# Optimization experiments

Hardware: AMD Instinct MI355X
Metric: run time of the kernel (lower is better)

The kernel has to match this reference:

```python
import jax, jax.numpy as jnp
import numpy as np

FS = 50000000.0
PI = jnp.pi


def _scale_matrix(alpha, kW, n_pad):
    """kW x kW matrix equal to torch linear-interp (align_corners=False)
    kW -> N -> kW with N = round(kW / clamp(alpha, 0.001)), N bounded by n_pad."""
    a = jnp.maximum(alpha, 0.001)
    N = jnp.clip(jnp.round(kW / a), 1, n_pad).astype(jnp.int32)
    Nf = N.astype(jnp.float32)
    eye_k = jnp.eye(kW, dtype=jnp.float32)
    eye_n = jnp.eye(n_pad, dtype=jnp.float32)
    # down-sample matrix D: length kW -> N (rows j >= N masked to 0)
    j = jnp.arange(n_pad, dtype=jnp.float32)
    c = jnp.maximum((j + 0.5) * (kW / Nf) - 0.5, 0.0)
    i0f = jnp.floor(c)
    w1 = c - i0f
    i0 = jnp.clip(i0f.astype(jnp.int32), 0, kW - 1)
    i1 = jnp.minimum(i0 + 1, kW - 1)
    D = (1.0 - w1)[:, None] * eye_k[i0] + w1[:, None] * eye_k[i1]
    D = D * (jnp.arange(n_pad) < N)[:, None]
    # up-sample matrix U: length N -> kW (reads only cols < N)
    i = jnp.arange(kW, dtype=jnp.float32)
    c2 = jnp.maximum((i + 0.5) * (Nf / kW) - 0.5, 0.0)
    j0 = jnp.floor(c2).astype(jnp.int32)
    j1 = jnp.minimum(j0 + 1, N - 1)
    w2 = c2 - j0.astype(jnp.float32)
    U = (1.0 - w2)[:, None] * eye_n[j0] + w2[:, None] * eye_n[j1]
    return U @ D  # [kW, kW]


def _mix_phase(w, phi):
    # w: [B,OC,2,1,kW], phi: [B,kW]; complex rotation of (I,Q) channel pair
    I, Q = w[:, :, 0, 0, :], w[:, :, 1, 0, :]
    c, sn = jnp.cos(phi)[:, None, :], jnp.sin(phi)[:, None, :]
    return jnp.stack([I * c - Q * sn, I * sn + Q * c], axis=2)[:, :, :, None, :]


def _steered_kernels(z, s, base_w, B):
    OC, IC, _, kW = base_w.shape
    n_pad = 2 * kW
    sf = jnp.nan_to_num(s)
    act = z > 0
    pick = lambda idx, neutral: jnp.where(act[:, idx], sf[:, idx], neutral)
    wB = jnp.broadcast_to(base_w[None], (B, OC, IC, 1, kW))
    # SCALE (PERTURB_ORDER idx 1)
    alpha = pick(1, 1.0)
    M = jax.vmap(lambda a: _scale_matrix(a, kW, n_pad))(alpha)  # [B,kW,kW]
    wB = jnp.einsum('bij,bocuj->bocui', M, wB)
    # CFO (idx 0) then CHIRP (idx 4): sequential phase rotations = summed phase
    n = jnp.arange(kW, dtype=jnp.float32)
    phi = 2.0 * PI * pick(0, 0.0)[:, None] * n[None, :] / FS
    t = n / FS
    phi = phi + PI * pick(4, 0.0)[:, None] * (t ** 2)[None, :]
    wB = _mix_phase(wB, phi)
    # GAIN (idx 2)
    wB = pick(2, 1.0)[:, None, None, None, None] * wB
    # SHIFT (idx 3): per-sample circular roll, out[i] = in[(i - s) mod kW]
    sh = jnp.round(pick(3, 0.0)).astype(jnp.int32)
    idx = (jnp.arange(kW)[None, :] - sh[:, None]) % kW  # [B,kW]
    idx = jnp.broadcast_to(idx[:, None, None, None, :], wB.shape)
    wB = jnp.take_along_axis(wB, idx, axis=-1)
    return wB  # [B,OC,2,1,kW]


def reference(x, z, s, base_w):
    B, IC, _, L = x.shape
    OC, _, _, kW = base_w.shape
    wB = _steered_kernels(z, s, base_w, B)
    xG = x.reshape(1, B * IC, 1, L)
    wG = wB.reshape(B * OC, IC, 1, kW)
    y = jax.lax.conv_general_dilated(
        xG, wG, window_strides=(1, 1), padding=[(0, 0), (kW // 2, kW // 2)],
        dimension_numbers=('NCHW', 'OIHW', 'NCHW'), feature_group_count=B)
    return y.reshape(B, OC, 1, L)


def setup_inputs() -> dict:
    key = jax.random.key(0)
    ks = jax.random.split(key, 4)
    B, OC, IC, kW, L = 32, 64, 2, 65, 65536
    x = jax.random.normal(ks[0], (B, IC, 1, L), dtype=jnp.float32)
    base_w = jax.random.normal(ks[1], (OC, IC, 1, kW), dtype=jnp.float32) * 0.1
    z = jax.random.randint(ks[2], (B, 5), 0, 2).astype(jnp.int32)
    u = jax.random.uniform(ks[3], (B, 5), dtype=jnp.float32)
    f0 = (u[:, 0] * 2.0 - 1.0) * 1.0e5         # CFO in +/-100 kHz
    alpha = 0.75 + u[:, 1] * 0.65               # SCALE in [0.75, 1.4]
    gain = 0.5 + u[:, 2]                        # GAIN in [0.5, 1.5]
    shift = jnp.round((u[:, 3] * 2.0 - 1.0) * 3.0)  # SHIFT integer in [-3, 3]
    chirp = (u[:, 4] * 2.0 - 1.0) * 1.0e12      # CHIRP rate
    s = jnp.stack([f0, alpha, gain, shift, chirp], axis=1)
    return {"x": x, "z": z, "s": s, "base_w": base_w}
```

## Files before the change

kernel.cpp:

```cpp
#include <hip/hip_runtime.h>
#include <math.h>

#define KW 65
#define L_LEN 65536
#define B_N 32
#define OC_N 64
#define KPAD 160
#define SEC 80
#define LT 256
#define NT 4
#define LGRP (LT*NT)
#define XBASE 344

typedef __attribute__((ext_vector_type(8))) short short8;
typedef __attribute__((ext_vector_type(4))) float f32x4;

__device__ __forceinline__ unsigned short f2bf(float f) {
    unsigned u = __builtin_bit_cast(unsigned, f);
    unsigned r = u + 0x7FFFu + ((u >> 16) & 1u);
    return (unsigned short)(r >> 16);
}

__device__ __forceinline__ float nan0(float v) {
    if (isnan(v)) return 0.0f;
    if (isinf(v)) return v > 0.0f ? 3.4028234663852886e38f : -3.4028234663852886e38f;
    return v;
}

__global__ __launch_bounds__(256) void steer_weights(
        const int* __restrict__ z, const float* __restrict__ s,
        const float* __restrict__ bw, unsigned short* __restrict__ wpk) {
    const float PI = 3.14159265358979323846f;
    const float FS = 50000000.0f;
    int b = blockIdx.x;
    int t = threadIdx.x;

    const int*   zb = z + b * 5;
    const float* sb = s + b * 5;
    float f0    = (zb[0] > 0) ? nan0(sb[0]) : 0.0f;
    float alpha = (zb[1] > 0) ? nan0(sb[1]) : 1.0f;
    float gain  = (zb[2] > 0) ? nan0(sb[2]) : 1.0f;
    float shf   = (zb[3] > 0) ? nan0(sb[3]) : 0.0f;
    float chirp = (zb[4] > 0) ? nan0(sb[4]) : 0.0f;

    float a = fmaxf(alpha, 0.001f);
    float Nf_raw = rintf(65.0f / a);
    int   N  = (int)fminf(fmaxf(Nf_raw, 1.0f), 130.0f);
    float Nf = (float)N;
    int   sh = (int)rintf(shf);

    __shared__ float rw[OC_N][2][KW];
    __shared__ float cph[KW], sph[KW];
    __shared__ int   j0t[KW], j1t[KW];
    __shared__ float w2t[KW];
    __shared__ int   i0t[130], i1t[130];
    __shared__ float w1t[130];

    if (t < KW) {
        float n  = (float)t;
        float tt = n / FS;
        float phi = 2.0f * PI * f0 * n / FS + PI * chirp * tt * tt;
        cph[t] = cosf(phi);
        sph[t] = sinf(phi);
        float c2  = fmaxf(((float)t + 0.5f) * (Nf / 65.0f) - 0.5f, 0.0f);
        float j0f = floorf(c2);
        j0t[t] = (int)j0f;
        j1t[t] = min((int)j0f + 1, N - 1);
        w2t[t] = c2 - j0f;
    } else if (t < KW + 130) {
        int j = t - KW;
        float c   = fmaxf(((float)j + 0.5f) * (65.0f / Nf) - 0.5f, 0.0f);
        float i0f = floorf(c);
        int   i0  = min((int)i0f, KW - 1);
        i0t[j] = i0;
        i1t[j] = min(i0 + 1, KW - 1);
        w1t[j] = c - i0f;
    }
    __syncthreads();

    for (int item = t; item < 128 * KW; item += 256) {
        int row = item / KW, i = item % KW;
        const float* w = bw + row * KW;
        int j0 = j0t[i], j1 = j1t[i];
        float v0 = (1.0f - w1t[j0]) * w[i0t[j0]] + w1t[j0] * w[i1t[j0]];
        float v1 = (1.0f - w1t[j1]) * w[i0t[j1]] + w1t[j1] * w[i1t[j1]];
        rw[row >> 1][row & 1][i] = (1.0f - w2t[i]) * v0 + w2t[i] * v1;
    }
    __syncthreads();

    {
        int oc = t >> 2, q = t & 3;
        unsigned short* ob = wpk + ((size_t)b * OC_N + oc) * KPAD;
        int sh0 = ((sh % KW) + KW) % KW;
        int k0 = 17 * q, k1 = min(KW, k0 + 17);
        for (int k = k0; k < k1; ++k) {
            float I = rw[oc][0][k], Q = rw[oc][1][k];
            float cp = cph[k], sp = sph[k];
            float Ip = (I * cp - Q * sp) * gain;
            float Qp = (I * sp + Q * cp) * gain;
            int kk = k + sh0; if (kk >= KW) kk -= KW;
            ob[kk]       = f2bf(Ip);
            ob[SEC + kk] = f2bf(Qp);
        }
        if (q == 3) {
            for (int kk = KW; kk < SEC; ++kk) { ob[kk] = 0; ob[SEC + kk] = 0; }
        }
    }
}

__global__ __launch_bounds__(256, 3) void steer_conv_mfma(
        const float* __restrict__ x, const unsigned short* __restrict__ wpk,
        float* __restrict__ y) {
    int b   = blockIdx.y;
    int L0  = blockIdx.x * LGRP;
    int tid = threadIdx.x;
    int wv = tid >> 6, lane = tid & 63;
    int c = lane & 15, g = lane >> 4;
    int a = wv & 1, lsub = wv >> 1;

    __shared__ __align__(16) unsigned short xt[2][8][2][XBASE];

    short8 afr[2][5];
    #pragma unroll
    for (int ot = 0; ot < 2; ++ot) {
        const unsigned short* wb = wpk + ((size_t)b * OC_N + 32 * a + 16 * ot + c) * KPAD;
        #pragma unroll
        for (int s = 0; s < 5; ++s)
            afr[ot][s] = *(const short8*)(wb + 32 * s + 8 * g);
    }

    const float* xb = x + (size_t)b * 2 * L_LEN;

    bool isLoader = (tid >= 84);
    int lidx = tid - 84;
    int lch = lidx / 86, li4 = lidx % 86;

    int boff[5];
    #pragma unroll
    for (int s = 0; s < 5; ++s) {
        int k0 = 32 * s + 8 * g;
        int ch = (k0 >= SEC) ? 1 : 0;
        int t0 = k0 - SEC * ch;
        boff[s] = ch * XBASE + 128 * lsub + 8 * c + t0;
    }

    float4 v;
    if (isLoader) {
        int gi = L0 - 32 + 4 * li4;
        if (gi >= 0 && gi + 3 < L_LEN) {
            v = *(const float4*)(xb + (size_t)lch * L_LEN + gi);
        } else {
            float tmp[4];
            #pragma unroll
            for (int u = 0; u < 4; ++u) {
                int q = gi + u;
                tmp[u] = (q >= 0 && q < L_LEN) ? xb[(size_t)lch * L_LEN + q] : 0.0f;
            }
            v = make_float4(tmp[0], tmp[1], tmp[2], tmp[3]);
        }
    }

    int cur = 0;
    for (int t = 0; t < NT; ++t) {
        int l0 = L0 + t * LT;
        if (isLoader) {
            unsigned r0 = (unsigned)f2bf(v.x) | ((unsigned)f2bf(v.y) << 16);
            unsigned r1 = (unsigned)f2bf(v.z) | ((unsigned)f2bf(v.w) << 16);
            *(uint2*)&xt[cur][0][lch][4 * li4] = make_uint2(r0, r1);
        }
        __syncthreads();
        if (tid < 84) {
            int ch = tid / 42, j = tid % 42;
            const unsigned* src = (const unsigned*)&xt[cur][0][ch][8 * j];
            unsigned d[8];
            #pragma unroll
            for (int i = 0; i < 8; ++i) d[i] = src[i];
            #pragma unroll
            for (int p = 1; p < 8; ++p) {
                int q = p >> 1;
                unsigned o[4];
                #pragma unroll
                for (int i = 0; i < 4; ++i)
                    o[i] = (p & 1) ? ((d[i + q] >> 16) | (d[i + q + 1] << 16)) : d[i + q];
                *(uint4*)&xt[cur][p][ch][8 * j] = make_uint4(o[0], o[1], o[2], o[3]);
            }
        } else if (t + 1 < NT) {
            int gi = L0 + (t + 1) * LT - 32 + 4 * li4;
            if (gi >= 0 && gi + 3 < L_LEN) {
                v = *(const float4*)(xb + (size_t)lch * L_LEN + gi);
            } else {
                float tmp[4];
                #pragma unroll
                for (int u = 0; u < 4; ++u) {
                    int q = gi + u;
                    tmp[u] = (q >= 0 && q < L_LEN) ? xb[(size_t)lch * L_LEN + q] : 0.0f;
                }
                v = make_float4(tmp[0], tmp[1], tmp[2], tmp[3]);
            }
        }
        __syncthreads();

        f32x4 acc[2][8];
        #pragma unroll
        for (int ot = 0; ot < 2; ++ot)
            #pragma unroll
            for (int p = 0; p < 8; ++p) acc[ot][p] = (f32x4){0.f, 0.f, 0.f, 0.f};

        #pragma unroll
        for (int p = 0; p < 8; ++p) {
            const unsigned short* xp = &xt[cur][p][0][0];
            #pragma unroll
            for (int s = 0; s < 5; ++s) {
                short8 bfr = *(const short8*)(xp + boff[s]);
                acc[0][p] = __builtin_amdgcn_mfma_f32_16x16x32_bf16(afr[0][s], bfr, acc[0][p], 0, 0, 0);
                acc[1][p] = __builtin_amdgcn_mfma_f32_16x16x32_bf16(afr[1][s], bfr, acc[1][p], 0, 0, 0);
            }
        }

        #pragma unroll
        for (int ot = 0; ot < 2; ++ot) {
            #pragma unroll
            for (int r = 0; r < 4; ++r) {
                int oc = 32 * a + 16 * ot + 4 * g + r;
                float* yr = y + ((size_t)b * OC_N + oc) * L_LEN + l0 + 128 * lsub + 8 * c;
                f32x4 lo = { acc[ot][0][r], acc[ot][1][r], acc[ot][2][r], acc[ot][3][r] };
                f32x4 hi = { acc[ot][4][r], acc[ot][5][r], acc[ot][6][r], acc[ot][7][r] };
                *(f32x4*)yr       = lo;
                *((f32x4*)yr + 1) = hi;
            }
        }
        cur ^= 1;
    }
}

extern "C" void kernel_launch(void* const* d_in, const int* in_sizes, int n_in,
                              void* d_out, int out_size, void* d_ws, size_t ws_size,
                              hipStream_t stream) {
    const float* x  = (const float*)d_in[0];
    const int*   z  = (const int*)d_in[1];
    const float* s  = (const float*)d_in[2];
    const float* bw = (const float*)d_in[3];
    float* y = (float*)d_out;
    unsigned short* wpk = (unsigned short*)d_ws;

    steer_weights<<<dim3(B_N), dim3(256), 0, stream>>>(z, s, bw, wpk);
    steer_conv_mfma<<<dim3(L_LEN / LGRP, B_N), dim3(256), 0, stream>>>(x, wpk, y);
}
```

Before: 142.2 us.

## Build shifted bf16 conv windows in registers instead of eight LDS copies

The conv kernel no longer stages eight pre-shifted copies of the input tile in shared memory. Each lane now loads two 16-byte chunks per K-slice and builds all eight shifted B fragments in registers with shifts and ORs. This drops the second barrier and the specialised shifter threads, and cuts LDS use enough to possibly raise occupancy. NT also doubles to 8, so each block handles twice the L range and there are half as many blocks. The cost is more VALU work and register pressure per MFMA, and fewer blocks to fill the GPU.

```diff
diff --git a/kernel.cpp b/kernel.cpp
--- a/kernel.cpp
+++ b/kernel.cpp
@@ -8,12 +8,13 @@
 #define KPAD 160
 #define SEC 80
 #define LT 256
-#define NT 4
+#define NT 8
 #define LGRP (LT*NT)
 #define XBASE 344
 
 typedef __attribute__((ext_vector_type(8))) short short8;
 typedef __attribute__((ext_vector_type(4))) float f32x4;
+typedef __attribute__((ext_vector_type(4))) unsigned u32x4;
 
 __device__ __forceinline__ unsigned short f2bf(float f) {
     unsigned u = __builtin_bit_cast(unsigned, f);
@@ -118,7 +119,7 @@
     int c = lane & 15, g = lane >> 4;
     int a = wv & 1, lsub = wv >> 1;
 
-    __shared__ __align__(16) unsigned short xt[2][8][2][XBASE];
+    __shared__ __align__(16) unsigned short xt[2][2][XBASE];
 
     short8 afr[2][5];
     #pragma unroll
@@ -131,9 +132,8 @@
 
     const float* xb = x + (size_t)b * 2 * L_LEN;
 
-    bool isLoader = (tid >= 84);
-    int lidx = tid - 84;
-    int lch = lidx / 86, li4 = lidx % 86;
+    bool isLdr = (tid < 172);
+    int lch = tid / 86, li4 = tid % 86;
 
     int boff[5];
     #pragma unroll
@@ -144,9 +144,9 @@
         boff[s] = ch * XBASE + 128 * lsub + 8 * c + t0;
     }
 
-    float4 v;
-    if (isLoader) {
-        int gi = L0 - 32 + 4 * li4;
+    auto loadwin = [&](int l0) -> float4 {
+        int gi = l0 - 32 + 4 * li4;
+        float4 v;
         if (gi >= 0 && gi + 3 < L_LEN) {
             v = *(const float4*)(xb + (size_t)lch * L_LEN + gi);
         } else {
@@ -158,60 +158,51 @@
             }
             v = make_float4(tmp[0], tmp[1], tmp[2], tmp[3]);
         }
-    }
+        return v;
+    };
+
+    float4 v = make_float4(0.f, 0.f, 0.f, 0.f);
+    if (isLdr) v = loadwin(L0);
 
     int cur = 0;
     for (int t = 0; t < NT; ++t) {
         int l0 = L0 + t * LT;
-        if (isLoader) {
+        if (isLdr) {
             unsigned r0 = (unsigned)f2bf(v.x) | ((unsigned)f2bf(v.y) << 16);
             unsigned r1 = (unsigned)f2bf(v.z) | ((unsigned)f2bf(v.w) << 16);
-            *(uint2*)&xt[cur][0][lch][4 * li4] = make_uint2(r0, r1);
+            *(uint2*)&xt[cur][lch][4 * li4] = make_uint2(r0, r1);
         }
         __syncthreads();
-        if (tid < 84) {
-            int ch = tid / 42, j = tid % 42;
-            const unsigned* src = (const unsigned*)&xt[cur][0][ch][8 * j];
-            unsigned d[8];
-            #pragma unroll
-            for (int i = 0; i < 8; ++i) d[i] = src[i];
-            #pragma unroll
-            for (int p = 1; p < 8; ++p) {
-                int q = p >> 1;
-                unsigned o[4];
-                #pragma unroll
-                for (int i = 0; i < 4; ++i)
-                    o[i] = (p & 1) ? ((d[i + q] >> 16) | (d[i + q + 1] << 16)) : d[i + q];
-                *(uint4*)&xt[cur][p][ch][8 * j] = make_uint4(o[0], o[1], o[2], o[3]);
-            }
-        } else if (t + 1 < NT) {
-            int gi = L0 + (t + 1) * LT - 32 + 4 * li4;
-            if (gi >= 0 && gi + 3 < L_LEN) {
-                v = *(const float4*)(xb + (size_t)lch * L_LEN + gi);
-            } else {
-                float tmp[4];
-                #pragma unroll
-                for (int u = 0; u < 4; ++u) {
-                    int q = gi + u;
-                    tmp[u] = (q >= 0 && q < L_LEN) ? xb[(size_t)lch * L_LEN + q] : 0.0f;
+
+        float4 vN = v;
+        if (isLdr && t + 1 < NT) vN = loadwin(l0 + LT);
+
+        f32x4 acc[2][8];
+        #pragma unroll
+        for (int ot = 0; ot < 2; ++ot)
+            #pragma unroll
+            for (int p = 0; p < 8; ++p) acc[ot][p] = (f32x4){0.f, 0.f, 0.f, 0.f};
+
+        const unsigned short* xs = &xt[cur][0][0];
+        #pragma unroll
+        for (int s = 0; s < 5; ++s) {
+            const uint4* w16 = (const uint4*)(xs + boff[s]);
+            uint4 q0 = w16[0], q1 = w16[1];
+            unsigned d[8] = { q0.x, q0.y, q0.z, q0.w, q1.x, q1.y, q1.z, q1.w };
+            #pragma unroll
+            for (int p = 0; p < 8; ++p) {
+                u32x4 ov;
+                if (p & 1) {
+                    int q = p >> 1;
+                    ov = (u32x4){ (d[q]     >> 16) | (d[q + 1] << 16),
+                                  (d[q + 1] >> 16) | (d[q + 2] << 16),
+                                  (d[q + 2] >> 16) | (d[q + 3] << 16),
+                                  (d[q + 3] >> 16) | (d[q + 4] << 16) };
+                } else {
+                    int q = p >> 1;
+                    ov = (u32x4){ d[q], d[q + 1], d[q + 2], d[q + 3] };
                 }
-                v = make_float4(tmp[0], tmp[1], tmp[2], tmp[3]);
-            }
-        }
-        __syncthreads();
-
-        f32x4 acc[2][8];
-        #pragma unroll
-        for (int ot = 0; ot < 2; ++ot)
-            #pragma unroll
-            for (int p = 0; p < 8; ++p) acc[ot][p] = (f32x4){0.f, 0.f, 0.f, 0.f};
-
-        #pragma unroll
-        for (int p = 0; p < 8; ++p) {
-            const unsigned short* xp = &xt[cur][p][0][0];
-            #pragma unroll
-            for (int s = 0; s < 5; ++s) {
-                short8 bfr = *(const short8*)(xp + boff[s]);
+                short8 bfr = __builtin_bit_cast(short8, ov);
                 acc[0][p] = __builtin_amdgcn_mfma_f32_16x16x32_bf16(afr[0][s], bfr, acc[0][p], 0, 0, 0);
                 acc[1][p] = __builtin_amdgcn_mfma_f32_16x16x32_bf16(afr[1][s], bfr, acc[1][p], 0, 0, 0);
             }
@@ -229,6 +220,7 @@
                 *((f32x4*)yr + 1) = hi;
             }
         }
+        v = vN;
         cur ^= 1;
     }
 }
```

Result: slower. 201.7 us (+41.9%).

## Parallelize weight steering over OC groups and streamline conv tile pipeline

Applied to the files above, without the earlier changes.

The weight-steering kernel is split across 8 output-channel groups per batch, so it runs on 256 blocks instead of 32. In the conv kernel each loader thread now builds all eight shifted bf16 copies directly from registers. This removes the separate shift pass and one __syncthreads per tile, and the next tile's global load is issued before the MFMA work. Output stores are split into two halves, issued mid-compute, and each block covers twice as many tiles. The cost is fewer conv blocks, which may hurt load balance, plus more register pressure in the loader threads.

```diff
diff --git a/kernel.cpp b/kernel.cpp
--- a/kernel.cpp
+++ b/kernel.cpp
@@ -8,7 +8,7 @@
 #define KPAD 160
 #define SEC 80
 #define LT 256
-#define NT 4
+#define NT 8
 #define LGRP (LT*NT)
 #define XBASE 344
 
@@ -19,6 +19,10 @@
     unsigned u = __builtin_bit_cast(unsigned, f);
     unsigned r = u + 0x7FFFu + ((u >> 16) & 1u);
     return (unsigned short)(r >> 16);
+}
+
+__device__ __forceinline__ unsigned pk2(float a, float b) {
+    return (unsigned)f2bf(a) | ((unsigned)f2bf(b) << 16);
 }
 
 __device__ __forceinline__ float nan0(float v) {
@@ -32,8 +36,9 @@
         const float* __restrict__ bw, unsigned short* __restrict__ wpk) {
     const float PI = 3.14159265358979323846f;
     const float FS = 50000000.0f;
-    int b = blockIdx.x;
-    int t = threadIdx.x;
+    int ocg = blockIdx.x;
+    int b   = blockIdx.y;
+    int t   = threadIdx.x;
 
     const int*   zb = z + b * 5;
     const float* sb = s + b * 5;
@@ -49,7 +54,7 @@
     float Nf = (float)N;
     int   sh = (int)rintf(shf);
 
-    __shared__ float rw[OC_N][2][KW];
+    __shared__ float rw[8][2][KW];
     __shared__ float cph[KW], sph[KW];
     __shared__ int   j0t[KW], j1t[KW];
     __shared__ float w2t[KW];
@@ -78,9 +83,9 @@
     }
     __syncthreads();
 
-    for (int item = t; item < 128 * KW; item += 256) {
+    for (int item = t; item < 16 * KW; item += 256) {
         int row = item / KW, i = item % KW;
-        const float* w = bw + row * KW;
+        const float* w = bw + (((ocg * 8 + (row >> 1)) * 2) + (row & 1)) * KW;
         int j0 = j0t[i], j1 = j1t[i];
         float v0 = (1.0f - w1t[j0]) * w[i0t[j0]] + w1t[j0] * w[i1t[j0]];
         float v1 = (1.0f - w1t[j1]) * w[i0t[j1]] + w1t[j1] * w[i1t[j1]];
@@ -88,23 +93,23 @@
     }
     __syncthreads();
 
-    {
-        int oc = t >> 2, q = t & 3;
-        unsigned short* ob = wpk + ((size_t)b * OC_N + oc) * KPAD;
-        int sh0 = ((sh % KW) + KW) % KW;
-        int k0 = 17 * q, k1 = min(KW, k0 + 17);
-        for (int k = k0; k < k1; ++k) {
-            float I = rw[oc][0][k], Q = rw[oc][1][k];
-            float cp = cph[k], sp = sph[k];
-            float Ip = (I * cp - Q * sp) * gain;
-            float Qp = (I * sp + Q * cp) * gain;
-            int kk = k + sh0; if (kk >= KW) kk -= KW;
-            ob[kk]       = f2bf(Ip);
-            ob[SEC + kk] = f2bf(Qp);
-        }
-        if (q == 3) {
-            for (int kk = KW; kk < SEC; ++kk) { ob[kk] = 0; ob[SEC + kk] = 0; }
-        }
+    int sh0 = ((sh % KW) + KW) % KW;
+    for (int item = t; item < 8 * KW; item += 256) {
+        int ocl = item / KW, k = item % KW;
+        unsigned short* ob = wpk + ((size_t)b * OC_N + ocg * 8 + ocl) * KPAD;
+        float I = rw[ocl][0][k], Q = rw[ocl][1][k];
+        float cp = cph[k], sp = sph[k];
+        float Ip = (I * cp - Q * sp) * gain;
+        float Qp = (I * sp + Q * cp) * gain;
+        int kk = k + sh0; if (kk >= KW) kk -= KW;
+        ob[kk]       = f2bf(Ip);
+        ob[SEC + kk] = f2bf(Qp);
+    }
+    for (int item = t; item < 8 * 30; item += 256) {
+        int ocl = item / 30, rem = item % 30;
+        int sec = rem / 15, kk = KW + rem % 15;
+        unsigned short* ob = wpk + ((size_t)b * OC_N + ocg * 8 + ocl) * KPAD;
+        ob[sec * SEC + kk] = 0;
     }
 }
 
@@ -131,9 +136,8 @@
 
     const float* xb = x + (size_t)b * 2 * L_LEN;
 
-    bool isLoader = (tid >= 84);
-    int lidx = tid - 84;
-    int lch = lidx / 86, li4 = lidx % 86;
+    bool isLdr = (tid < 86);
+    int lch = tid / 43, lj = tid % 43;
 
     int boff[5];
     #pragma unroll
@@ -144,61 +148,58 @@
         boff[s] = ch * XBASE + 128 * lsub + 8 * c + t0;
     }
 
-    float4 v;
-    if (isLoader) {
-        int gi = L0 - 32 + 4 * li4;
-        if (gi >= 0 && gi + 3 < L_LEN) {
-            v = *(const float4*)(xb + (size_t)lch * L_LEN + gi);
-        } else {
-            float tmp[4];
-            #pragma unroll
-            for (int u = 0; u < 4; ++u) {
-                int q = gi + u;
-                tmp[u] = (q >= 0 && q < L_LEN) ? xb[(size_t)lch * L_LEN + q] : 0.0f;
-            }
-            v = make_float4(tmp[0], tmp[1], tmp[2], tmp[3]);
-        }
+    auto ldf4 = [&](int gi) -> float4 {
+        if (gi >= 0 && gi + 3 < L_LEN)
+            return *(const float4*)(xb + (size_t)lch * L_LEN + gi);
+        float tmp[4];
+        #pragma unroll
+        for (int u = 0; u < 4; ++u) {
+            int q = gi + u;
+            tmp[u] = (q >= 0 && q < L_LEN) ? xb[(size_t)lch * L_LEN + q] : 0.0f;
+        }
+        return make_float4(tmp[0], tmp[1], tmp[2], tmp[3]);
+    };
+
+    float4 w4[4];
+    #pragma unroll
+    for (int k = 0; k < 4; ++k) w4[k] = make_float4(0.f, 0.f, 0.f, 0.f);
+    if (isLdr) {
+        int gi0 = L0 - 32 + 8 * lj;
+        #pragma unroll
+        for (int k = 0; k < 4; ++k) w4[k] = ldf4(gi0 + 4 * k);
     }
 
     int cur = 0;
     for (int t = 0; t < NT; ++t) {
         int l0 = L0 + t * LT;
-        if (isLoader) {
-            unsigned r0 = (unsigned)f2bf(v.x) | ((unsigned)f2bf(v.y) << 16);
-            unsigned r1 = (unsigned)f2bf(v.z) | ((unsigned)f2bf(v.w) << 16);
-            *(uint2*)&xt[cur][0][lch][4 * li4] = make_uint2(r0, r1);
+        if (isLdr) {
+            unsigned u[8];
+            #pragma unroll
+            for (int k = 0; k < 4; ++k) {
+                u[2 * k]     = pk2(w4[k].x, w4[k].y);
+                u[2 * k + 1] = pk2(w4[k].z, w4[k].w);
+            }
+            #pragma unroll
+            for (int p = 0; p < 8; ++p) {
+                int q = p >> 1;
+                uint4 o;
+                if (p & 1)
+                    o = make_uint4((u[q]     >> 16) | (u[q + 1] << 16),
+                                   (u[q + 1] >> 16) | (u[q + 2] << 16),
+                                   (u[q + 2] >> 16) | (u[q + 3] << 16),
+                                   (u[q + 3] >> 16) | (u[q + 4] << 16));
+                else
+                    o = make_uint4(u[q], u[q + 1], u[q + 2], u[q + 3]);
+                *(uint4*)&xt[cur][p][lch][8 * lj] = o;
+            }
         }
         __syncthreads();
-        if (tid < 84) {
-            int ch = tid / 42, j = tid % 42;
-            const unsigned* src = (const unsigned*)&xt[cur][0][ch][8 * j];
-            unsigned d[8];
-            #pragma unroll
-            for (int i = 0; i < 8; ++i) d[i] = src[i];
-            #pragma unroll
-            for (int p = 1; p < 8; ++p) {
-                int q = p >> 1;
-                unsigned o[4];
-                #pragma unroll
-                for (int i = 0; i < 4; ++i)
-                    o[i] = (p & 1) ? ((d[i + q] >> 16) | (d[i + q + 1] << 16)) : d[i + q];
-                *(uint4*)&xt[cur][p][ch][8 * j] = make_uint4(o[0], o[1], o[2], o[3]);
-            }
-        } else if (t + 1 < NT) {
-            int gi = L0 + (t + 1) * LT - 32 + 4 * li4;
-            if (gi >= 0 && gi + 3 < L_LEN) {
-                v = *(const float4*)(xb + (size_t)lch * L_LEN + gi);
-            } else {
-                float tmp[4];
-                #pragma unroll
-                for (int u = 0; u < 4; ++u) {
-                    int q = gi + u;
-                    tmp[u] = (q >= 0 && q < L_LEN) ? xb[(size_t)lch * L_LEN + q] : 0.0f;
-                }
-                v = make_float4(tmp[0], tmp[1], tmp[2], tmp[3]);
-            }
-        }
-        __syncthreads();
+
+        if (isLdr && t + 1 < NT) {
+            int gi0 = l0 + LT - 32 + 8 * lj;
+            #pragma unroll
+            for (int k = 0; k < 4; ++k) w4[k] = ldf4(gi0 + 4 * k);
+        }
 
         f32x4 acc[2][8];
         #pragma unroll
@@ -215,18 +216,25 @@
                 acc[0][p] = __builtin_amdgcn_mfma_f32_16x16x32_bf16(afr[0][s], bfr, acc[0][p], 0, 0, 0);
                 acc[1][p] = __builtin_amdgcn_mfma_f32_16x16x32_bf16(afr[1][s], bfr, acc[1][p], 0, 0, 0);
             }
-        }
-
-        #pragma unroll
-        for (int ot = 0; ot < 2; ++ot) {
-            #pragma unroll
-            for (int r = 0; r < 4; ++r) {
-                int oc = 32 * a + 16 * ot + 4 * g + r;
-                float* yr = y + ((size_t)b * OC_N + oc) * L_LEN + l0 + 128 * lsub + 8 * c;
-                f32x4 lo = { acc[ot][0][r], acc[ot][1][r], acc[ot][2][r], acc[ot][3][r] };
-                f32x4 hi = { acc[ot][4][r], acc[ot][5][r], acc[ot][6][r], acc[ot][7][r] };
-                *(f32x4*)yr       = lo;
-                *((f32x4*)yr + 1) = hi;
+            if (p == 3) {
+                #pragma unroll
+                for (int ot = 0; ot < 2; ++ot)
+                    #pragma unroll
+                    for (int r = 0; r < 4; ++r) {
+                        int oc = 32 * a + 16 * ot + 4 * g + r;
+                        float* yr = y + ((size_t)b * OC_N + oc) * L_LEN + l0 + 128 * lsub + 8 * c;
+                        *(f32x4*)yr = (f32x4){ acc[ot][0][r], acc[ot][1][r], acc[ot][2][r], acc[ot][3][r] };
+                    }
+            }
+            if (p == 7) {
+                #pragma unroll
+                for (int ot = 0; ot < 2; ++ot)
+                    #pragma unroll
+                    for (int r = 0; r < 4; ++r) {
+                        int oc = 32 * a + 16 * ot + 4 * g + r;
+                        float* yr = y + ((size_t)b * OC_N + oc) * L_LEN + l0 + 128 * lsub + 8 * c + 4;
+                        *(f32x4*)yr = (f32x4){ acc[ot][4][r], acc[ot][5][r], acc[ot][6][r], acc[ot][7][r] };
+                    }
             }
         }
         cur ^= 1;
@@ -243,6 +251,6 @@
     float* y = (float*)d_out;
     unsigned short* wpk = (unsigned short*)d_ws;
 
-    steer_weights<<<dim3(B_N), dim3(256), 0, stream>>>(z, s, bw, wpk);
+    steer_weights<<<dim3(8, B_N), dim3(256), 0, stream>>>(z, s, bw, wpk);
     steer_conv_mfma<<<dim3(L_LEN / LGRP, B_N), dim3(256), 0, stream>>>(x, wpk, y);
 }
```

Measured after the change: 273.8 us. +92.6%, slower.
